# Performance work log

Measured on AMD Instinct MI355X. Metric: run time of the kernel, lower is better.

Reference implementation:

```python
import jax, jax.numpy as jnp
import numpy as np

B, S = 2048, 512
OUT, EMB, ENC, DEC = 1, 16, 32, 32


def setup_inputs() -> dict:
    key = jax.random.key(0)
    ks = jax.random.split(key, 14)
    f = lambda k, shape: jax.random.normal(k, shape, dtype=jnp.float32) * 0.05
    return {
        "dec_in": f(ks[0], (B, OUT)),
        "s": f(ks[1], (B, DEC)),
        "enc_out": f(ks[2], (S, B, 2 * ENC)),
        # Bahdanau attention params: Linear(2*ENC+DEC -> DEC), v: Linear(DEC -> 1, no bias)
        "W_attn": f(ks[3], (DEC, 2 * ENC + DEC)),
        "b_attn": f(ks[4], (DEC,)),
        "v_attn": f(ks[5], (DEC,)),
        # embedding Linear(OUT -> EMB)
        "W_emb": f(ks[6], (EMB, OUT)),
        "b_emb": f(ks[7], (EMB,)),
        # GRU: input size 2*ENC+EMB = 80, hidden DEC = 32 (torch gate order r,z,n)
        "W_ih": f(ks[8], (3 * DEC, 2 * ENC + EMB)),
        "W_hh": f(ks[9], (3 * DEC, DEC)),
        "b_ih": f(ks[10], (3 * DEC,)),
        "b_hh": f(ks[11], (3 * DEC,)),
        # fc Linear(DEC + 2*ENC + EMB = 112 -> OUT)
        "W_fc": f(ks[12], (OUT, 2 * ENC + DEC + EMB)),
        "b_fc": f(ks[13], (OUT,)),
    }


def reference(dec_in, s, enc_out, W_attn, b_attn, v_attn, W_emb, b_emb,
              W_ih, W_hh, b_ih, b_hh, W_fc, b_fc):
    enc_bse = jnp.transpose(enc_out, (1, 0, 2))  # (B, S, 2*ENC)
    Bn, Sn = enc_bse.shape[0], enc_bse.shape[1]
    # Bahdanau attention: tanh(Linear([s; enc_out])) @ v, softmax over seq
    s_rep = jnp.broadcast_to(s[:, None, :], (Bn, Sn, s.shape[1]))
    energy = jnp.tanh(jnp.concatenate([s_rep, enc_bse], axis=-1) @ W_attn.T + b_attn)  # (B,S,DEC)
    att = jax.nn.softmax(energy @ v_attn, axis=1)  # (B, S)
    # context = bmm(att, enc_out)
    ctx = jnp.einsum('bs,bsh->bh', att, enc_bse)  # (B, 2*ENC)
    # embedding MLP (dropout = identity in eval)
    emb = jax.nn.relu(dec_in @ W_emb.T + b_emb)  # (B, EMB)
    # single GRU step (torch gate order: r, z, n)
    x = jnp.concatenate([emb, ctx], axis=-1)  # (B, 2*ENC+EMB)
    gi = x @ W_ih.T + b_ih
    gh = s @ W_hh.T + b_hh
    H = s.shape[1]
    r = jax.nn.sigmoid(gi[:, :H] + gh[:, :H])
    z = jax.nn.sigmoid(gi[:, H:2 * H] + gh[:, H:2 * H])
    n = jnp.tanh(gi[:, 2 * H:] + r * gh[:, 2 * H:])
    h_new = (1.0 - z) * n + z * s  # (B, DEC); also dec_out for single step
    # output projection on [dec_out; ctx; embedded]
    pred = jnp.concatenate([h_new, ctx, emb], axis=-1) @ W_fc.T + b_fc  # (B, OUT)
    return pred, h_new
```

## Files before the change

### kernel.cpp

```cpp
#include <hip/hip_runtime.h>

typedef __attribute__((ext_vector_type(8))) short short8;
typedef __attribute__((ext_vector_type(4))) float f32x4;

__device__ __forceinline__ short f2bf(float f) {
    __bf16 h = (__bf16)f;
    return (short)__builtin_bit_cast(unsigned short, h);
}

__device__ __forceinline__ float fast_tanh(float x) {
    float e2 = __expf(2.f * x);
    return 1.f - 2.f * __builtin_amdgcn_rcpf(e2 + 1.f);
}

__device__ __forceinline__ float fast_sigmoid(float x) {
    return __builtin_amdgcn_rcpf(1.f + __expf(-x));
}

__global__ __launch_bounds__(256, 2) void attn_kernel(
        const float* __restrict__ enc, const float* __restrict__ s_in,
        const float* __restrict__ W_attn, const float* __restrict__ b_attn,
        const float* __restrict__ v_attn,
        float* __restrict__ ctx_part, float* __restrict__ l_part,
        int NS, int chunk) {
    const int tid  = threadIdx.x;
    const int lane = tid & 63;
    const int w    = tid >> 6;
    const int cid  = blockIdx.x % NS;
    const int btile = (blockIdx.x / NS) * 4 + w;
    const int b0 = btile * 16;
    const int lo = lane & 15;
    const int g  = lane >> 4;

    short8 bW2[2][2];
    f32x4 spre[2];
    float v0[4], v1[4];
    {
        const float* sp = s_in + (size_t)(b0 + lo) * 32 + 8 * g;
        float4 sa = *(const float4*)sp;
        float4 sb = *(const float4*)(sp + 4);
        short8 aS;
        aS[0]=f2bf(sa.x); aS[1]=f2bf(sa.y); aS[2]=f2bf(sa.z); aS[3]=f2bf(sa.w);
        aS[4]=f2bf(sb.x); aS[5]=f2bf(sb.y); aS[6]=f2bf(sb.z); aS[7]=f2bf(sb.w);
#pragma unroll
        for (int t = 0; t < 2; ++t) {
            const float* wp = W_attn + (size_t)(16*t + lo) * 96 + 8 * g;
            float4 wa = *(const float4*)wp;
            float4 wb = *(const float4*)(wp + 4);
            short8 bW1;
            bW1[0]=f2bf(wa.x); bW1[1]=f2bf(wa.y); bW1[2]=f2bf(wa.z); bW1[3]=f2bf(wa.w);
            bW1[4]=f2bf(wb.x); bW1[5]=f2bf(wb.y); bW1[6]=f2bf(wb.z); bW1[7]=f2bf(wb.w);
            f32x4 ci;
#pragma unroll
            for (int j = 0; j < 4; ++j) ci[j] = b_attn[16*t + 4*g + j];
            spre[t] = __builtin_amdgcn_mfma_f32_16x16x32_bf16(bW1, aS, ci, 0, 0, 0);
#pragma unroll
            for (int cc = 0; cc < 2; ++cc) {
                const float* qp = W_attn + (size_t)(16*t + lo) * 96 + 32 + 32*cc + 8*g;
                float4 qa = *(const float4*)qp;
                float4 qb = *(const float4*)(qp + 4);
                short8 bb;
                bb[0]=f2bf(qa.x); bb[1]=f2bf(qa.y); bb[2]=f2bf(qa.z); bb[3]=f2bf(qa.w);
                bb[4]=f2bf(qb.x); bb[5]=f2bf(qb.y); bb[6]=f2bf(qb.z); bb[7]=f2bf(qb.w);
                bW2[t][cc] = bb;
            }
        }
#pragma unroll
        for (int j = 0; j < 4; ++j) { v0[j] = v_attn[4*g + j]; v1[j] = v_attn[16 + 4*g + j]; }
    }

    float ctx[16];
#pragma unroll
    for (int i = 0; i < 16; ++i) ctx[i] = 0.f;
    float l_acc = 0.f;

    const size_t rowstride = (size_t)2048 * 64;
    const float* pc = enc + (size_t)(cid * chunk) * rowstride + (size_t)(b0 + lo) * 64 + 8 * g;

    float4 r0a,r0b,r0c,r0d, r1a,r1b,r1c,r1d, r2a,r2b,r2c,r2d, r3a,r3b,r3c,r3d;
#define LOAD_ENC(P, A,Bq,C,D) { const float4* q = (const float4*)(P); A = q[0]; Bq = q[1]; C = q[8]; D = q[9]; }

#define BODY(A,Bq,C,D) { \
    short8 a0, a1; \
    a0[0]=f2bf(A.x); a0[1]=f2bf(A.y); a0[2]=f2bf(A.z); a0[3]=f2bf(A.w); \
    a0[4]=f2bf(Bq.x); a0[5]=f2bf(Bq.y); a0[6]=f2bf(Bq.z); a0[7]=f2bf(Bq.w); \
    a1[0]=f2bf(C.x); a1[1]=f2bf(C.y); a1[2]=f2bf(C.z); a1[3]=f2bf(C.w); \
    a1[4]=f2bf(D.x); a1[5]=f2bf(D.y); a1[6]=f2bf(D.z); a1[7]=f2bf(D.w); \
    f32x4 acc0 = __builtin_amdgcn_mfma_f32_16x16x32_bf16(bW2[0][0], a0, spre[0], 0,0,0); \
    acc0 = __builtin_amdgcn_mfma_f32_16x16x32_bf16(bW2[0][1], a1, acc0, 0,0,0); \
    f32x4 acc1 = __builtin_amdgcn_mfma_f32_16x16x32_bf16(bW2[1][0], a0, spre[1], 0,0,0); \
    acc1 = __builtin_amdgcn_mfma_f32_16x16x32_bf16(bW2[1][1], a1, acc1, 0,0,0); \
    float part = fast_tanh(acc0[0])*v0[0] + fast_tanh(acc0[1])*v0[1] \
               + fast_tanh(acc0[2])*v0[2] + fast_tanh(acc0[3])*v0[3] \
               + fast_tanh(acc1[0])*v1[0] + fast_tanh(acc1[1])*v1[1] \
               + fast_tanh(acc1[2])*v1[2] + fast_tanh(acc1[3])*v1[3]; \
    part += __shfl_xor(part, 16); \
    part += __shfl_xor(part, 32); \
    float w_ = __expf(part); \
    l_acc += w_; \
    ctx[0] += w_*A.x;  ctx[1] += w_*A.y;  ctx[2] += w_*A.z;  ctx[3] += w_*A.w; \
    ctx[4] += w_*Bq.x; ctx[5] += w_*Bq.y; ctx[6] += w_*Bq.z; ctx[7] += w_*Bq.w; \
    ctx[8] += w_*C.x;  ctx[9] += w_*C.y;  ctx[10] += w_*C.z; ctx[11] += w_*C.w; \
    ctx[12] += w_*D.x; ctx[13] += w_*D.y; ctx[14] += w_*D.z; ctx[15] += w_*D.w; \
}

    LOAD_ENC(pc + 0*rowstride, r0a, r0b, r0c, r0d);
    LOAD_ENC(pc + 1*rowstride, r1a, r1b, r1c, r1d);
    LOAD_ENC(pc + 2*rowstride, r2a, r2b, r2c, r2d);
    LOAD_ENC(pc + 3*rowstride, r3a, r3b, r3c, r3d);
    for (int i = 0; i < chunk - 4; i += 4) {
        BODY(r0a, r0b, r0c, r0d);  LOAD_ENC(pc + 4*rowstride, r0a, r0b, r0c, r0d);
        BODY(r1a, r1b, r1c, r1d);  LOAD_ENC(pc + 5*rowstride, r1a, r1b, r1c, r1d);
        BODY(r2a, r2b, r2c, r2d);  LOAD_ENC(pc + 6*rowstride, r2a, r2b, r2c, r2d);
        BODY(r3a, r3b, r3c, r3d);  LOAD_ENC(pc + 7*rowstride, r3a, r3b, r3c, r3d);
        pc += 4 * rowstride;
    }
    BODY(r0a, r0b, r0c, r0d);
    BODY(r1a, r1b, r1c, r1d);
    BODY(r2a, r2b, r2c, r2d);
    BODY(r3a, r3b, r3c, r3d);
#undef BODY
#undef LOAD_ENC

    float* cp = ctx_part + (size_t)(cid * 2048 + b0 + lo) * 64 + 8 * g;
    *(float4*)(cp)      = make_float4(ctx[0],  ctx[1],  ctx[2],  ctx[3]);
    *(float4*)(cp + 4)  = make_float4(ctx[4],  ctx[5],  ctx[6],  ctx[7]);
    *(float4*)(cp + 32) = make_float4(ctx[8],  ctx[9],  ctx[10], ctx[11]);
    *(float4*)(cp + 36) = make_float4(ctx[12], ctx[13], ctx[14], ctx[15]);
    if (lane < 16) l_part[cid * 2048 + b0 + lane] = l_acc;
}

__global__ __launch_bounds__(256) void finish_kernel(
        const float* __restrict__ dec_in, const float* __restrict__ s_in,
        const float* __restrict__ W_emb, const float* __restrict__ b_emb,
        const float* __restrict__ W_ih, const float* __restrict__ W_hh,
        const float* __restrict__ b_ih, const float* __restrict__ b_hh,
        const float* __restrict__ W_fc, const float* __restrict__ b_fc,
        const float* __restrict__ ctx_part, const float* __restrict__ l_part,
        float* __restrict__ out, int NS) {
    __shared__ __align__(16) float x_lds[8][80];
    __shared__ __align__(16) float s_lds[8][32];
    const int tid = threadIdx.x;
    const int bl = tid >> 5;
    const int h  = tid & 31;
    const int b  = blockIdx.x * 8 + bl;

    float c0 = 0.f, c1 = 0.f, ls = 0.f;
    for (int c = 0; c < NS; ++c) {
        const float* cp = ctx_part + (size_t)(c * 2048 + b) * 64;
        c0 += cp[h];
        c1 += cp[h + 32];
        ls += l_part[c * 2048 + b];
    }
    float inv = 1.f / ls;
    x_lds[bl][16 + h] = c0 * inv;
    x_lds[bl][48 + h] = c1 * inv;
    if (h < 16) x_lds[bl][h] = fmaxf(0.f, dec_in[b] * W_emb[h] + b_emb[h]);
    s_lds[bl][h] = s_in[b * 32 + h];
    __syncthreads();

    float a_r  = b_ih[h]      + b_hh[h];
    float a_z  = b_ih[32 + h] + b_hh[32 + h];
    float gi_n = b_ih[64 + h];
    float gh_n = b_hh[64 + h];
    const float4* xv4 = (const float4*)&x_lds[bl][0];
    const float4* wr4 = (const float4*)(W_ih + 80 * h);
    const float4* wz4 = (const float4*)(W_ih + 80 * (32 + h));
    const float4* wn4 = (const float4*)(W_ih + 80 * (64 + h));
#pragma unroll
    for (int j = 0; j < 20; ++j) {
        float4 x = xv4[j], wr = wr4[j], wz = wz4[j], wn = wn4[j];
        a_r  += x.x*wr.x + x.y*wr.y + x.z*wr.z + x.w*wr.w;
        a_z  += x.x*wz.x + x.y*wz.y + x.z*wz.z + x.w*wz.w;
        gi_n += x.x*wn.x + x.y*wn.y + x.z*wn.z + x.w*wn.w;
    }
    const float4* sv4 = (const float4*)&s_lds[bl][0];
    const float4* hr4 = (const float4*)(W_hh + 32 * h);
    const float4* hz4 = (const float4*)(W_hh + 32 * (32 + h));
    const float4* hn4 = (const float4*)(W_hh + 32 * (64 + h));
#pragma unroll
    for (int j = 0; j < 8; ++j) {
        float4 x = sv4[j], wr = hr4[j], wz = hz4[j], wn = hn4[j];
        a_r  += x.x*wr.x + x.y*wr.y + x.z*wr.z + x.w*wr.w;
        a_z  += x.x*wz.x + x.y*wz.y + x.z*wz.z + x.w*wz.w;
        gh_n += x.x*wn.x + x.y*wn.y + x.z*wn.z + x.w*wn.w;
    }
    float r = fast_sigmoid(a_r);
    float z = fast_sigmoid(a_z);
    float n = fast_tanh(gi_n + r * gh_n);
    float sv = s_lds[bl][h];
    float hn = (1.f - z) * n + z * sv;
    out[2048 + b * 32 + h] = hn;

    float p = hn * W_fc[h] + x_lds[bl][16 + h] * W_fc[32 + h] + x_lds[bl][48 + h] * W_fc[64 + h];
    if (h < 16) p += x_lds[bl][h] * W_fc[96 + h];
    p += __shfl_xor(p, 1); p += __shfl_xor(p, 2); p += __shfl_xor(p, 4);
    p += __shfl_xor(p, 8); p += __shfl_xor(p, 16);
    if (h == 0) out[b] = p + b_fc[0];
}

extern "C" void kernel_launch(void* const* d_in, const int* in_sizes, int n_in,
                              void* d_out, int out_size, void* d_ws, size_t ws_size,
                              hipStream_t stream) {
    const float* dec_in = (const float*)d_in[0];
    const float* s_in   = (const float*)d_in[1];
    const float* enc    = (const float*)d_in[2];
    const float* W_attn = (const float*)d_in[3];
    const float* b_attn = (const float*)d_in[4];
    const float* v_attn = (const float*)d_in[5];
    const float* W_emb  = (const float*)d_in[6];
    const float* b_emb  = (const float*)d_in[7];
    const float* W_ih   = (const float*)d_in[8];
    const float* W_hh   = (const float*)d_in[9];
    const float* b_ih   = (const float*)d_in[10];
    const float* b_hh   = (const float*)d_in[11];
    const float* W_fc   = (const float*)d_in[12];
    const float* b_fc   = (const float*)d_in[13];
    float* out = (float*)d_out;

    int NS = 16;
    while (NS > 1 && (size_t)NS * (2048u * 64u + 2048u) * sizeof(float) > ws_size) NS >>= 1;
    int chunk = 512 / NS;
    float* ctx_part = (float*)d_ws;
    float* l_part   = ctx_part + (size_t)NS * 2048 * 64;

    attn_kernel<<<dim3(32 * NS), dim3(256), 0, stream>>>(
        enc, s_in, W_attn, b_attn, v_attn, ctx_part, l_part, NS, chunk);
    finish_kernel<<<dim3(256), dim3(256), 0, stream>>>(
        dec_in, s_in, W_emb, b_emb, W_ih, W_hh, b_ih, b_hh, W_fc, b_fc,
        ctx_part, l_part, out, NS);
}
```

Before: 61.43 us.

## Stage encoder rows through swizzled LDS with fully coalesced global loads

Each wave now loads its 16x64 encoder tile per sequence step as contiguous float4s across the lane index (fully coalesced), writes it into a per-wave double-buffered, XOR-swizzled LDS slab, and reads back the MFMA operand layout from LDS. A three-deep register prefetch pipeline overlaps global loads with compute. This targets uncoalesced/strided global access in the memory-bound attention pass. In exchange it adds LDS traffic (32 KB per block, which may limit occupancy) and relies on wave-local ordering without explicit barriers.

```diff
diff --git a/kernel.cpp b/kernel.cpp
--- a/kernel.cpp
+++ b/kernel.cpp
@@ -25,12 +25,16 @@
         int NS, int chunk) {
     const int tid  = threadIdx.x;
     const int lane = tid & 63;
-    const int w    = tid >> 6;
+    const int wv   = tid >> 6;
     const int cid  = blockIdx.x % NS;
-    const int btile = (blockIdx.x / NS) * 4 + w;
+    const int btile = (blockIdx.x / NS) * 4 + wv;
     const int b0 = btile * 16;
     const int lo = lane & 15;
     const int g  = lane >> 4;
+
+    __shared__ __align__(16) float lds_all[4][2][1024];
+    float* const sl0 = &lds_all[wv][0][0];
+    float* const sl1 = &lds_all[wv][1][0];
 
     short8 bW2[2][2];
     f32x4 spre[2];
@@ -75,17 +79,47 @@
     float l_acc = 0.f;
 
     const size_t rowstride = (size_t)2048 * 64;
-    const float* pc = enc + (size_t)(cid * chunk) * rowstride + (size_t)(b0 + lo) * 64 + 8 * g;
-
-    float4 r0a,r0b,r0c,r0d, r1a,r1b,r1c,r1d, r2a,r2b,r2c,r2d, r3a,r3b,r3c,r3d;
-#define LOAD_ENC(P, A,Bq,C,D) { const float4* q = (const float4*)(P); A = q[0]; Bq = q[1]; C = q[8]; D = q[9]; }
-
-#define BODY(A,Bq,C,D) { \
+    const float* pc = enc + (size_t)(cid * chunk) * rowstride + (size_t)b0 * 64;
+
+    const int lhi = lane >> 4;
+    const int w_off0 = (0*256 + lane*4) ^ ((((0*4)+lhi)&7)<<2);
+    const int w_off1 = (1*256 + lane*4) ^ ((((1*4)+lhi)&7)<<2);
+    const int w_off2 = (2*256 + lane*4) ^ ((((2*4)+lhi)&7)<<2);
+    const int w_off3 = (3*256 + lane*4) ^ ((((3*4)+lhi)&7)<<2);
+    const int rsw = (lo & 7) << 2;
+    const int r_offA = (lo*64 + g*8     ) ^ rsw;
+    const int r_offB = (lo*64 + g*8 +  4) ^ rsw;
+    const int r_offC = (lo*64 + g*8 + 32) ^ rsw;
+    const int r_offD = (lo*64 + g*8 + 36) ^ rsw;
+
+    float4 b0_0,b0_1,b0_2,b0_3, b1_0,b1_1,b1_2,b1_3,
+           b2_0,b2_1,b2_2,b2_3, b3_0,b3_1,b3_2,b3_3;
+    float4 tA, tB, tC, tD;
+
+#define GLOAD(B, ROW) { const float* q = pc + (size_t)(ROW) * rowstride; \
+    B##_0 = *(const float4*)(q +        lane*4); \
+    B##_1 = *(const float4*)(q +  256 + lane*4); \
+    B##_2 = *(const float4*)(q +  512 + lane*4); \
+    B##_3 = *(const float4*)(q +  768 + lane*4); }
+
+#define SWRITE(SL, B) { \
+    *(float4*)((SL) + w_off0) = B##_0; \
+    *(float4*)((SL) + w_off1) = B##_1; \
+    *(float4*)((SL) + w_off2) = B##_2; \
+    *(float4*)((SL) + w_off3) = B##_3; }
+
+#define SREAD(SL) { \
+    tA = *(const float4*)((SL) + r_offA); \
+    tB = *(const float4*)((SL) + r_offB); \
+    tC = *(const float4*)((SL) + r_offC); \
+    tD = *(const float4*)((SL) + r_offD); }
+
+#define BODY() { \
     short8 a0, a1; \
-    a0[0]=f2bf(A.x); a0[1]=f2bf(A.y); a0[2]=f2bf(A.z); a0[3]=f2bf(A.w); \
-    a0[4]=f2bf(Bq.x); a0[5]=f2bf(Bq.y); a0[6]=f2bf(Bq.z); a0[7]=f2bf(Bq.w); \
-    a1[0]=f2bf(C.x); a1[1]=f2bf(C.y); a1[2]=f2bf(C.z); a1[3]=f2bf(C.w); \
-    a1[4]=f2bf(D.x); a1[5]=f2bf(D.y); a1[6]=f2bf(D.z); a1[7]=f2bf(D.w); \
+    a0[0]=f2bf(tA.x); a0[1]=f2bf(tA.y); a0[2]=f2bf(tA.z); a0[3]=f2bf(tA.w); \
+    a0[4]=f2bf(tB.x); a0[5]=f2bf(tB.y); a0[6]=f2bf(tB.z); a0[7]=f2bf(tB.w); \
+    a1[0]=f2bf(tC.x); a1[1]=f2bf(tC.y); a1[2]=f2bf(tC.z); a1[3]=f2bf(tC.w); \
+    a1[4]=f2bf(tD.x); a1[5]=f2bf(tD.y); a1[6]=f2bf(tD.z); a1[7]=f2bf(tD.w); \
     f32x4 acc0 = __builtin_amdgcn_mfma_f32_16x16x32_bf16(bW2[0][0], a0, spre[0], 0,0,0); \
     acc0 = __builtin_amdgcn_mfma_f32_16x16x32_bf16(bW2[0][1], a1, acc0, 0,0,0); \
     f32x4 acc1 = __builtin_amdgcn_mfma_f32_16x16x32_bf16(bW2[1][0], a0, spre[1], 0,0,0); \
@@ -98,29 +132,29 @@
     part += __shfl_xor(part, 32); \
     float w_ = __expf(part); \
     l_acc += w_; \
-    ctx[0] += w_*A.x;  ctx[1] += w_*A.y;  ctx[2] += w_*A.z;  ctx[3] += w_*A.w; \
-    ctx[4] += w_*Bq.x; ctx[5] += w_*Bq.y; ctx[6] += w_*Bq.z; ctx[7] += w_*Bq.w; \
-    ctx[8] += w_*C.x;  ctx[9] += w_*C.y;  ctx[10] += w_*C.z; ctx[11] += w_*C.w; \
-    ctx[12] += w_*D.x; ctx[13] += w_*D.y; ctx[14] += w_*D.z; ctx[15] += w_*D.w; \
-}
-
-    LOAD_ENC(pc + 0*rowstride, r0a, r0b, r0c, r0d);
-    LOAD_ENC(pc + 1*rowstride, r1a, r1b, r1c, r1d);
-    LOAD_ENC(pc + 2*rowstride, r2a, r2b, r2c, r2d);
-    LOAD_ENC(pc + 3*rowstride, r3a, r3b, r3c, r3d);
-    for (int i = 0; i < chunk - 4; i += 4) {
-        BODY(r0a, r0b, r0c, r0d);  LOAD_ENC(pc + 4*rowstride, r0a, r0b, r0c, r0d);
-        BODY(r1a, r1b, r1c, r1d);  LOAD_ENC(pc + 5*rowstride, r1a, r1b, r1c, r1d);
-        BODY(r2a, r2b, r2c, r2d);  LOAD_ENC(pc + 6*rowstride, r2a, r2b, r2c, r2d);
-        BODY(r3a, r3b, r3c, r3d);  LOAD_ENC(pc + 7*rowstride, r3a, r3b, r3c, r3d);
-        pc += 4 * rowstride;
-    }
-    BODY(r0a, r0b, r0c, r0d);
-    BODY(r1a, r1b, r1c, r1d);
-    BODY(r2a, r2b, r2c, r2d);
-    BODY(r3a, r3b, r3c, r3d);
+    ctx[0] += w_*tA.x;  ctx[1] += w_*tA.y;  ctx[2] += w_*tA.z;  ctx[3] += w_*tA.w; \
+    ctx[4] += w_*tB.x;  ctx[5] += w_*tB.y;  ctx[6] += w_*tB.z;  ctx[7] += w_*tB.w; \
+    ctx[8] += w_*tC.x;  ctx[9] += w_*tC.y;  ctx[10] += w_*tC.z; ctx[11] += w_*tC.w; \
+    ctx[12] += w_*tD.x; ctx[13] += w_*tD.y; ctx[14] += w_*tD.z; ctx[15] += w_*tD.w; \
+}
+
+    GLOAD(b0, 0); GLOAD(b1, 1); GLOAD(b2, 2);
+    SWRITE(sl0, b0);
+    int i = 0;
+    for (; i + 7 < chunk; i += 4) {
+        SREAD(sl0); SWRITE(sl1, b1); GLOAD(b3, i+3); BODY();
+        SREAD(sl1); SWRITE(sl0, b2); GLOAD(b0, i+4); BODY();
+        SREAD(sl0); SWRITE(sl1, b3); GLOAD(b1, i+5); BODY();
+        SREAD(sl1); SWRITE(sl0, b0); GLOAD(b2, i+6); BODY();
+    }
+    SREAD(sl0); SWRITE(sl1, b1); GLOAD(b3, i+3); BODY();
+    SREAD(sl1); SWRITE(sl0, b2); BODY();
+    SREAD(sl0); SWRITE(sl1, b3); BODY();
+    SREAD(sl1); BODY();
 #undef BODY
-#undef LOAD_ENC
+#undef SREAD
+#undef SWRITE
+#undef GLOAD
 
     float* cp = ctx_part + (size_t)(cid * 2048 + b0 + lo) * 64 + 8 * g;
     *(float4*)(cp)      = make_float4(ctx[0],  ctx[1],  ctx[2],  ctx[3]);
```

Result: no change. 61.80 us (+0.6%).

## Precompute s projection in separate kernel, double NS splits, shorten prefetch depth

Applied to the files above, without the earlier changes.

Moves the per-tile s·W_attn projection into a new small spre_kernel whose results the attention kernel loads from workspace. This shortens the attention kernel's prologue. The sequence split count rises from 16 to 32, doubling the grid to expose more parallelism at the cost of larger partial buffers for finish_kernel to reduce. The enc prefetch pipeline drops from four rows in flight to two to cut register pressure. That may expose more memory latency, and the extra kernel adds a launch.

```diff
diff --git a/kernel.cpp b/kernel.cpp
--- a/kernel.cpp
+++ b/kernel.cpp
@@ -17,57 +17,76 @@
     return __builtin_amdgcn_rcpf(1.f + __expf(-x));
 }
 
+__global__ __launch_bounds__(256) void spre_kernel(
+        const float* __restrict__ s_in, const float* __restrict__ W_attn,
+        const float* __restrict__ b_attn, float4* __restrict__ spre_all) {
+    const int tid = threadIdx.x;
+    const int lane = tid & 63;
+    const int wv = tid >> 6;
+    const int btile = blockIdx.x * 4 + wv;
+    const int b0 = btile * 16;
+    const int lo = lane & 15;
+    const int g  = lane >> 4;
+
+    const float* sp = s_in + (size_t)(b0 + lo) * 32 + 8 * g;
+    float4 sa = *(const float4*)sp;
+    float4 sb = *(const float4*)(sp + 4);
+    short8 aS;
+    aS[0]=f2bf(sa.x); aS[1]=f2bf(sa.y); aS[2]=f2bf(sa.z); aS[3]=f2bf(sa.w);
+    aS[4]=f2bf(sb.x); aS[5]=f2bf(sb.y); aS[6]=f2bf(sb.z); aS[7]=f2bf(sb.w);
+#pragma unroll
+    for (int t = 0; t < 2; ++t) {
+        const float* wp = W_attn + (size_t)(16*t + lo) * 96 + 8 * g;
+        float4 wa = *(const float4*)wp;
+        float4 wb = *(const float4*)(wp + 4);
+        short8 bW1;
+        bW1[0]=f2bf(wa.x); bW1[1]=f2bf(wa.y); bW1[2]=f2bf(wa.z); bW1[3]=f2bf(wa.w);
+        bW1[4]=f2bf(wb.x); bW1[5]=f2bf(wb.y); bW1[6]=f2bf(wb.z); bW1[7]=f2bf(wb.w);
+        f32x4 ci;
+#pragma unroll
+        for (int j = 0; j < 4; ++j) ci[j] = b_attn[16*t + 4*g + j];
+        f32x4 r = __builtin_amdgcn_mfma_f32_16x16x32_bf16(bW1, aS, ci, 0, 0, 0);
+        float4 o; o.x = r[0]; o.y = r[1]; o.z = r[2]; o.w = r[3];
+        spre_all[(btile * 2 + t) * 64 + lane] = o;
+    }
+}
+
 __global__ __launch_bounds__(256, 2) void attn_kernel(
-        const float* __restrict__ enc, const float* __restrict__ s_in,
-        const float* __restrict__ W_attn, const float* __restrict__ b_attn,
-        const float* __restrict__ v_attn,
+        const float* __restrict__ enc, const float* __restrict__ W_attn,
+        const float* __restrict__ v_attn, const float4* __restrict__ spre_all,
         float* __restrict__ ctx_part, float* __restrict__ l_part,
         int NS, int chunk) {
     const int tid  = threadIdx.x;
     const int lane = tid & 63;
-    const int w    = tid >> 6;
+    const int wv   = tid >> 6;
     const int cid  = blockIdx.x % NS;
-    const int btile = (blockIdx.x / NS) * 4 + w;
+    const int btile = (blockIdx.x / NS) * 4 + wv;
     const int b0 = btile * 16;
     const int lo = lane & 15;
     const int g  = lane >> 4;
 
     short8 bW2[2][2];
+#pragma unroll
+    for (int t = 0; t < 2; ++t)
+#pragma unroll
+        for (int cc = 0; cc < 2; ++cc) {
+            const float* qp = W_attn + (size_t)(16*t + lo) * 96 + 32 + 32*cc + 8*g;
+            float4 qa = *(const float4*)qp;
+            float4 qb = *(const float4*)(qp + 4);
+            short8 bb;
+            bb[0]=f2bf(qa.x); bb[1]=f2bf(qa.y); bb[2]=f2bf(qa.z); bb[3]=f2bf(qa.w);
+            bb[4]=f2bf(qb.x); bb[5]=f2bf(qb.y); bb[6]=f2bf(qb.z); bb[7]=f2bf(qb.w);
+            bW2[t][cc] = bb;
+        }
     f32x4 spre[2];
+#pragma unroll
+    for (int t = 0; t < 2; ++t) {
+        float4 o = spre_all[(btile * 2 + t) * 64 + lane];
+        spre[t][0] = o.x; spre[t][1] = o.y; spre[t][2] = o.z; spre[t][3] = o.w;
+    }
     float v0[4], v1[4];
-    {
-        const float* sp = s_in + (size_t)(b0 + lo) * 32 + 8 * g;
-        float4 sa = *(const float4*)sp;
-        float4 sb = *(const float4*)(sp + 4);
-        short8 aS;
-        aS[0]=f2bf(sa.x); aS[1]=f2bf(sa.y); aS[2]=f2bf(sa.z); aS[3]=f2bf(sa.w);
-        aS[4]=f2bf(sb.x); aS[5]=f2bf(sb.y); aS[6]=f2bf(sb.z); aS[7]=f2bf(sb.w);
-#pragma unroll
-        for (int t = 0; t < 2; ++t) {
-            const float* wp = W_attn + (size_t)(16*t + lo) * 96 + 8 * g;
-            float4 wa = *(const float4*)wp;
-            float4 wb = *(const float4*)(wp + 4);
-            short8 bW1;
-            bW1[0]=f2bf(wa.x); bW1[1]=f2bf(wa.y); bW1[2]=f2bf(wa.z); bW1[3]=f2bf(wa.w);
-            bW1[4]=f2bf(wb.x); bW1[5]=f2bf(wb.y); bW1[6]=f2bf(wb.z); bW1[7]=f2bf(wb.w);
-            f32x4 ci;
-#pragma unroll
-            for (int j = 0; j < 4; ++j) ci[j] = b_attn[16*t + 4*g + j];
-            spre[t] = __builtin_amdgcn_mfma_f32_16x16x32_bf16(bW1, aS, ci, 0, 0, 0);
-#pragma unroll
-            for (int cc = 0; cc < 2; ++cc) {
-                const float* qp = W_attn + (size_t)(16*t + lo) * 96 + 32 + 32*cc + 8*g;
-                float4 qa = *(const float4*)qp;
-                float4 qb = *(const float4*)(qp + 4);
-                short8 bb;
-                bb[0]=f2bf(qa.x); bb[1]=f2bf(qa.y); bb[2]=f2bf(qa.z); bb[3]=f2bf(qa.w);
-                bb[4]=f2bf(qb.x); bb[5]=f2bf(qb.y); bb[6]=f2bf(qb.z); bb[7]=f2bf(qb.w);
-                bW2[t][cc] = bb;
-            }
-        }
-#pragma unroll
-        for (int j = 0; j < 4; ++j) { v0[j] = v_attn[4*g + j]; v1[j] = v_attn[16 + 4*g + j]; }
-    }
+#pragma unroll
+    for (int j = 0; j < 4; ++j) { v0[j] = v_attn[4*g + j]; v1[j] = v_attn[16 + 4*g + j]; }
 
     float ctx[16];
 #pragma unroll
@@ -77,7 +96,7 @@
     const size_t rowstride = (size_t)2048 * 64;
     const float* pc = enc + (size_t)(cid * chunk) * rowstride + (size_t)(b0 + lo) * 64 + 8 * g;
 
-    float4 r0a,r0b,r0c,r0d, r1a,r1b,r1c,r1d, r2a,r2b,r2c,r2d, r3a,r3b,r3c,r3d;
+    float4 c0a,c0b,c1a,c1b, n0a,n0b,n1a,n1b;
 #define LOAD_ENC(P, A,Bq,C,D) { const float4* q = (const float4*)(P); A = q[0]; Bq = q[1]; C = q[8]; D = q[9]; }
 
 #define BODY(A,Bq,C,D) { \
@@ -104,21 +123,14 @@
     ctx[12] += w_*D.x; ctx[13] += w_*D.y; ctx[14] += w_*D.z; ctx[15] += w_*D.w; \
 }
 
-    LOAD_ENC(pc + 0*rowstride, r0a, r0b, r0c, r0d);
-    LOAD_ENC(pc + 1*rowstride, r1a, r1b, r1c, r1d);
-    LOAD_ENC(pc + 2*rowstride, r2a, r2b, r2c, r2d);
-    LOAD_ENC(pc + 3*rowstride, r3a, r3b, r3c, r3d);
-    for (int i = 0; i < chunk - 4; i += 4) {
-        BODY(r0a, r0b, r0c, r0d);  LOAD_ENC(pc + 4*rowstride, r0a, r0b, r0c, r0d);
-        BODY(r1a, r1b, r1c, r1d);  LOAD_ENC(pc + 5*rowstride, r1a, r1b, r1c, r1d);
-        BODY(r2a, r2b, r2c, r2d);  LOAD_ENC(pc + 6*rowstride, r2a, r2b, r2c, r2d);
-        BODY(r3a, r3b, r3c, r3d);  LOAD_ENC(pc + 7*rowstride, r3a, r3b, r3c, r3d);
-        pc += 4 * rowstride;
-    }
-    BODY(r0a, r0b, r0c, r0d);
-    BODY(r1a, r1b, r1c, r1d);
-    BODY(r2a, r2b, r2c, r2d);
-    BODY(r3a, r3b, r3c, r3d);
+    LOAD_ENC(pc, c0a, c0b, c1a, c1b);
+    for (int i = 0; i < chunk; i += 2) {
+        LOAD_ENC(pc + rowstride, n0a, n0b, n1a, n1b);
+        BODY(c0a, c0b, c1a, c1b);
+        if (i + 2 < chunk) { LOAD_ENC(pc + 2*rowstride, c0a, c0b, c1a, c1b); }
+        BODY(n0a, n0b, n1a, n1b);
+        pc += 2 * rowstride;
+    }
 #undef BODY
 #undef LOAD_ENC
 
@@ -218,14 +230,16 @@
     const float* b_fc   = (const float*)d_in[13];
     float* out = (float*)d_out;
 
-    int NS = 16;
-    while (NS > 1 && (size_t)NS * (2048u * 64u + 2048u) * sizeof(float) > ws_size) NS >>= 1;
+    int NS = 32;
+    while (NS > 1 && ((size_t)NS * (2048u * 64u + 2048u) + 128u * 2u * 64u * 4u) * sizeof(float) > ws_size) NS >>= 1;
     int chunk = 512 / NS;
     float* ctx_part = (float*)d_ws;
     float* l_part   = ctx_part + (size_t)NS * 2048 * 64;
-
+    float4* spre_all = (float4*)(l_part + (size_t)NS * 2048);
+
+    spre_kernel<<<dim3(32), dim3(256), 0, stream>>>(s_in, W_attn, b_attn, spre_all);
     attn_kernel<<<dim3(32 * NS), dim3(256), 0, stream>>>(
-        enc, s_in, W_attn, b_attn, v_attn, ctx_part, l_part, NS, chunk);
+        enc, W_attn, v_attn, spre_all, ctx_part, l_part, NS, chunk);
     finish_kernel<<<dim3(256), dim3(256), 0, stream>>>(
         dec_in, s_in, W_emb, b_emb, W_ih, W_hh, b_ih, b_hh, W_fc, b_fc,
         ctx_part, l_part, out, NS);
```

Measured after the change: 72.78 us. 18.5% more time.
